# Optimization experiments

Hardware: AMD Instinct MI355X
Metric: run time of the kernel (lower is better)

The kernel has to match this reference:

```python
import jax, jax.numpy as jnp
import numpy as np

D = 1024
H = 16
HD = D // H
EPS = 1e-9


def setup_inputs() -> dict:
    key = jax.random.key(0)
    ks = jax.random.split(key, 16)
    B, Lq, Lk = 8, 512, 1024
    s = 0.02
    return {
        "q": jax.random.normal(ks[0], (B, Lq, D), jnp.float32),
        "q_mask": jnp.ones((B, Lq), jnp.bool_),
        "kv": jax.random.normal(ks[1], (B, Lk, D), jnp.float32),
        "kv_mask": jnp.ones((B, Lk), jnp.bool_),
        # MultiheadAttention packed in-proj + out-proj
        "in_proj_w": jax.random.normal(ks[2], (3 * D, D), jnp.float32) * s,
        "in_proj_b": jnp.zeros((3 * D,), jnp.float32),
        "out_w": jax.random.normal(ks[3], (D, D), jnp.float32) * s,
        "out_b": jnp.zeros((D,), jnp.float32),
        # shared LayerNorm
        "ln_g": jnp.ones((D,), jnp.float32),
        "ln_b": jnp.zeros((D,), jnp.float32),
        # FFN
        "w1": jax.random.normal(ks[4], (4 * D, D), jnp.float32) * s,
        "b1": jnp.zeros((4 * D,), jnp.float32),
        "w2": jax.random.normal(ks[5], (D, 4 * D), jnp.float32) * s,
        "b2": jnp.zeros((D,), jnp.float32),
        # gate MLP
        "gw1": jax.random.normal(ks[6], (D, 2 * D), jnp.float32) * s,
        "gb1": jnp.zeros((D,), jnp.float32),
        "gw2": jax.random.normal(ks[7], (1, D), jnp.float32) * s,
        "gb2": jnp.zeros((1,), jnp.float32),
    }


def _layer_norm(x, g, b, eps=1e-5):
    mu = x.mean(-1, keepdims=True)
    var = ((x - mu) ** 2).mean(-1, keepdims=True)
    return (x - mu) * jax.lax.rsqrt(var + eps) * g + b


def reference(q, q_mask, kv, kv_mask, in_proj_w, in_proj_b, out_w, out_b,
              ln_g, ln_b, w1, b1, w2, b2, gw1, gb1, gw2, gb2):
    B, Lq, _ = q.shape
    Lk = kv.shape[1]
    # packed projections (torch Linear convention: x @ W.T + b)
    qp = (q @ in_proj_w[:D].T + in_proj_b[:D]).reshape(B, Lq, H, HD)
    kp = (kv @ in_proj_w[D:2 * D].T + in_proj_b[D:2 * D]).reshape(B, Lk, H, HD)
    vp = (kv @ in_proj_w[2 * D:].T + in_proj_b[2 * D:]).reshape(B, Lk, H, HD)
    scores = jnp.einsum('bqhd,bkhd->bhqk', qp, kp) / np.sqrt(HD)  # (B,H,Lq,Lk)
    scores = jnp.where(kv_mask[:, None, None, :], scores, -1e30)
    attn = jax.nn.softmax(scores, axis=-1)
    ctx = jnp.einsum('bhqk,bkhd->bqhd', attn, vp).reshape(B, Lq, D)
    attn_out = ctx @ out_w.T + out_b
    # entropy over keys, normalized by log(Lk), averaged over heads
    p = jnp.clip(attn, EPS)
    ent = -(p * jnp.log(p)).sum(-1) / jnp.log(jnp.float32(Lk))  # (B,H,Lq)
    ent = ent.mean(axis=1)[..., None]  # (B,Lq,1)
    conf = jnp.clip(1.0 - ent, 0.0, 1.0)
    # gate MLP on [q, attn_out]
    h = jax.nn.gelu(jnp.concatenate([q, attn_out], -1) @ gw1.T + gb1, approximate=False)
    g = jax.nn.sigmoid(h @ gw2.T + gb2) * conf
    q2 = _layer_norm(q + attn_out * g, ln_g, ln_b)
    ffn = jax.nn.gelu(q2 @ w1.T + b1, approximate=False) @ w2.T + b2
    q2 = _layer_norm(q2 + ffn, ln_g, ln_b)
    return q2, ent
```

## Files before the change

### kernel.cpp

```cpp
#include <hip/hip_runtime.h>
#include <cstdint>
#include <cstddef>

typedef __bf16 bf16;
typedef __bf16 bf16x8 __attribute__((ext_vector_type(8)));
typedef __bf16 bf16x4 __attribute__((ext_vector_type(4)));
typedef float  f32x4  __attribute__((ext_vector_type(4)));

#define GLOAD_LDS16(g, l) __builtin_amdgcn_global_load_lds( \
    (const __attribute__((address_space(1))) unsigned int*)(g), \
    (__attribute__((address_space(3))) unsigned int*)(l), 16, 0, 0)

static constexpr int D_  = 1024;
static constexpr int H_  = 16;
static constexpr int HD_ = 64;
static constexpr int B_  = 8;
static constexpr int LQ_ = 512;
static constexpr int LK_ = 1024;
static constexpr int MQ_ = B_ * LQ_;
static constexpr float LOG2E_ = 1.4426950408889634f;
static constexpr float INV_LN_LK_ = 0.14426950408889634f;
static constexpr float CSHIFT_ = 8.0f;

__device__ __forceinline__ float gelu_f(float v) {
    return 0.5f * v * (1.0f + erff(v * 0.70710678118654752f));
}

__global__ __launch_bounds__(256)
void cast_all_k(const float* __restrict__ ipw, const float* __restrict__ outw,
                const float* __restrict__ w1,  const float* __restrict__ w2,
                const float* __restrict__ gw1, const float* __restrict__ q,
                const float* __restrict__ kv,
                bf16* __restrict__ ipw_b, bf16* __restrict__ outw_b,
                bf16* __restrict__ w1_b,  bf16* __restrict__ w2_b,
                bf16* __restrict__ gw1_b, bf16* __restrict__ x_b,
                bf16* __restrict__ kv_b) {
    const int b = blockIdx.x, t = threadIdx.x;
    const float* src; bf16* dst; long e;
    if (b < 1536)       { src = ipw;  dst = ipw_b;  e = (long)b * 2048; }
    else if (b < 2048)  { src = outw; dst = outw_b; e = (long)(b - 1536) * 2048; }
    else if (b < 4096)  { src = w1;   dst = w1_b;   e = (long)(b - 2048) * 2048; }
    else if (b < 6144)  { src = w2;   dst = w2_b;   e = (long)(b - 4096) * 2048; }
    else if (b < 7168)  { src = gw1;  dst = gw1_b;  e = (long)(b - 6144) * 2048; }
    else if (b < 11264) { src = kv;   dst = kv_b;   e = (long)(b - 7168) * 2048; }
    else {
        long e2 = (long)(b - 11264) * 2048 + t * 8;
        float4 a = *(const float4*)(q + e2);
        float4 c = *(const float4*)(q + e2 + 4);
        bf16x8 o;
        o[0]=(bf16)a.x; o[1]=(bf16)a.y; o[2]=(bf16)a.z; o[3]=(bf16)a.w;
        o[4]=(bf16)c.x; o[5]=(bf16)c.y; o[6]=(bf16)c.z; o[7]=(bf16)c.w;
        long row = e2 >> 10, col = e2 & 1023;
        *(bf16x8*)(x_b + row * 2048 + col) = o;
        return;
    }
    e += t * 8;
    float4 a = *(const float4*)(src + e);
    float4 c = *(const float4*)(src + e + 4);
    bf16x8 o;
    o[0]=(bf16)a.x; o[1]=(bf16)a.y; o[2]=(bf16)a.z; o[3]=(bf16)a.w;
    o[4]=(bf16)c.x; o[5]=(bf16)c.y; o[6]=(bf16)c.z; o[7]=(bf16)c.w;
    *(bf16x8*)(dst + e) = o;
}

template<int ACT, int OUTB, int OUTF>
__device__ __forceinline__
void gemm_body(const bf16* __restrict__ A, int lda,
               const bf16* __restrict__ W, int ldw,
               const float* __restrict__ bias,
               bf16* __restrict__ Cb, int ldcb,
               float* __restrict__ Cf, int ldcf,
               int K) {
    __shared__ __attribute__((aligned(16))) bf16 As[128 * 32];
    __shared__ __attribute__((aligned(16))) bf16 Bs[128 * 32];
    const int gx = gridDim.x;
    const int nwg = gx * gridDim.y;
    const int flat = blockIdx.x + gx * blockIdx.y;
    const int swz = (flat & 7) * (nwg >> 3) + (flat >> 3);
    const int by = swz / gx, bx = swz - by * gx;
    const int t = threadIdx.x;
    const int w = t >> 6, l = t & 63;
    const int l15 = l & 15, lg = l >> 4;
    const int row0 = by * 128, col0 = bx * 128;
    const int wr = (w >> 1) * 64, wc = (w & 1) * 64;

    f32x4 acc[4][4];
#pragma unroll
    for (int m = 0; m < 4; ++m)
#pragma unroll
        for (int n = 0; n < 4; ++n) acc[m][n] = f32x4{0.f, 0.f, 0.f, 0.f};

    const int nk = K >> 5;
    for (int ks = 0; ks < nk; ++ks) {
        __syncthreads();
        const int k0 = ks * 32;
#pragma unroll
        for (int i = 0; i < 2; ++i) {
            int f = i * 256 + t;
            int rr = f >> 2, c8 = (f & 3) * 8;
            GLOAD_LDS16(A + (size_t)(row0 + rr) * lda + k0 + c8,
                        As + (size_t)(i * 256 + w * 64) * 8);
            GLOAD_LDS16(W + (size_t)(col0 + rr) * ldw + k0 + c8,
                        Bs + (size_t)(i * 256 + w * 64) * 8);
        }
        __syncthreads();
        bf16x8 af[4], bfm[4];
#pragma unroll
        for (int m = 0; m < 4; ++m)
            af[m] = *(const bf16x8*)&As[(wr + m * 16 + l15) * 32 + lg * 8];
#pragma unroll
        for (int n = 0; n < 4; ++n)
            bfm[n] = *(const bf16x8*)&Bs[(wc + n * 16 + l15) * 32 + lg * 8];
#pragma unroll
        for (int m = 0; m < 4; ++m)
#pragma unroll
            for (int n = 0; n < 4; ++n)
                acc[m][n] = __builtin_amdgcn_mfma_f32_16x16x32_bf16(af[m], bfm[n], acc[m][n], 0, 0, 0);
    }

#pragma unroll
    for (int n = 0; n < 4; ++n) {
        int gcol = col0 + wc + n * 16 + l15;
        float bv = bias ? bias[gcol] : 0.f;
#pragma unroll
        for (int m = 0; m < 4; ++m) {
            int grow = row0 + wr + m * 16 + lg * 4;
#pragma unroll
            for (int r = 0; r < 4; ++r) {
                float v = acc[m][n][r] + bv;
                if (ACT == 1) v = gelu_f(v);
                if (OUTB) Cb[(size_t)(grow + r) * ldcb + gcol] = (bf16)v;
                if (OUTF) Cf[(size_t)(grow + r) * ldcf + gcol] = v;
            }
        }
    }
}

__device__ __forceinline__
void gemm_splitk_body(const bf16* __restrict__ A, int lda,
                      const bf16* __restrict__ W, int ldw,
                      float* __restrict__ C0, float* __restrict__ C1, int ldcf,
                      int K, int aoff, int woff) {
    __shared__ __attribute__((aligned(16))) bf16 As[128 * 32];
    __shared__ __attribute__((aligned(16))) bf16 Bs[128 * 32];
    const int gx = gridDim.x, gy = gridDim.y;
    const int nwg = gx * gy * gridDim.z;
    const int flat = blockIdx.x + gx * (blockIdx.y + gy * blockIdx.z);
    const int swz = (flat & 7) * (nwg >> 3) + (flat >> 3);
    const int z = swz / (gx * gy);
    const int rem = swz - z * (gx * gy);
    const int by = rem / gx, bx = rem - by * gx;
    A += (size_t)z * aoff;
    W += (size_t)z * woff;
    float* Cf = z ? C1 : C0;

    const int t = threadIdx.x;
    const int w = t >> 6, l = t & 63;
    const int l15 = l & 15, lg = l >> 4;
    const int row0 = by * 128, col0 = bx * 128;
    const int wr = (w >> 1) * 64, wc = (w & 1) * 64;

    f32x4 acc[4][4];
#pragma unroll
    for (int m = 0; m < 4; ++m)
#pragma unroll
        for (int n = 0; n < 4; ++n) acc[m][n] = f32x4{0.f, 0.f, 0.f, 0.f};

    const int nk = K >> 5;
    for (int ks = 0; ks < nk; ++ks) {
        __syncthreads();
        const int k0 = ks * 32;
#pragma unroll
        for (int i = 0; i < 2; ++i) {
            int f = i * 256 + t;
            int rr = f >> 2, c8 = (f & 3) * 8;
            GLOAD_LDS16(A + (size_t)(row0 + rr) * lda + k0 + c8,
                        As + (size_t)(i * 256 + w * 64) * 8);
            GLOAD_LDS16(W + (size_t)(col0 + rr) * ldw + k0 + c8,
                        Bs + (size_t)(i * 256 + w * 64) * 8);
        }
        __syncthreads();
        bf16x8 af[4], bfm[4];
#pragma unroll
        for (int m = 0; m < 4; ++m)
            af[m] = *(const bf16x8*)&As[(wr + m * 16 + l15) * 32 + lg * 8];
#pragma unroll
        for (int n = 0; n < 4; ++n)
            bfm[n] = *(const bf16x8*)&Bs[(wc + n * 16 + l15) * 32 + lg * 8];
#pragma unroll
        for (int m = 0; m < 4; ++m)
#pragma unroll
            for (int n = 0; n < 4; ++n)
                acc[m][n] = __builtin_amdgcn_mfma_f32_16x16x32_bf16(af[m], bfm[n], acc[m][n], 0, 0, 0);
    }

#pragma unroll
    for (int n = 0; n < 4; ++n) {
        int gcol = col0 + wc + n * 16 + l15;
#pragma unroll
        for (int m = 0; m < 4; ++m) {
            int grow = row0 + wr + m * 16 + lg * 4;
#pragma unroll
            for (int r = 0; r < 4; ++r)
                Cf[(size_t)(grow + r) * ldcf + gcol] = acc[m][n][r];
        }
    }
}

__global__ __launch_bounds__(256)
void gemm_qproj_k(const bf16* A, const bf16* W, const float* bias, bf16* Cb) {
    gemm_body<0,1,0>(A, 2048, W, 1024, bias, Cb, 1024, nullptr, 0, 1024);
}
__global__ __launch_bounds__(256)
void gemm_kvproj_k(const bf16* A, const bf16* W, const float* bias, bf16* Cb) {
    gemm_body<0,1,0>(A, 1024, W, 1024, bias, Cb, 2048, nullptr, 0, 1024);
}
__global__ __launch_bounds__(256)
void gemm_outproj_k(const bf16* A, const bf16* W, const float* bias, bf16* Cb) {
    gemm_body<0,1,0>(A, 1024, W, 1024, bias, Cb, 2048, nullptr, 0, 1024);
}
__global__ __launch_bounds__(256)
void gemm_ffn1_k(const bf16* A, const bf16* W, const float* bias, bf16* Cb) {
    gemm_body<1,1,0>(A, 1024, W, 1024, bias, Cb, 4096, nullptr, 0, 1024);
}
__global__ __launch_bounds__(256)
void gemm_gate2_k(const bf16* A, const bf16* W, float* C0, float* C1) {
    gemm_splitk_body(A, 2048, W, 2048, C0, C1, 1024, 1024, 1024, 1024);
}
__global__ __launch_bounds__(256)
void gemm_ffn2_k(const bf16* A, const bf16* W, float* C0, float* C1) {
    gemm_splitk_body(A, 4096, W, 4096, C0, C1, 1024, 2048, 2048, 2048);
}

__device__ __forceinline__ float red16sum(float v) {
    v += __shfl_xor(v, 1, 64);
    v += __shfl_xor(v, 2, 64);
    v += __shfl_xor(v, 4, 64);
    v += __shfl_xor(v, 8, 64);
    return v;
}

__global__ __launch_bounds__(256)
void attn_k(const bf16* __restrict__ Qp, const bf16* __restrict__ KVp,
            bf16* __restrict__ ctx, float* __restrict__ entm) {
    __shared__ __attribute__((aligned(16))) bf16 Ks[64 * 72];
    __shared__ __attribute__((aligned(16))) bf16 Vts[64 * 72];
    __shared__ __attribute__((aligned(16))) bf16 Ps[4][16 * 72];
    const int t = threadIdx.x, w = t >> 6, l = t & 63;
    const int l15 = l & 15, lg = l >> 4;
    const int h = blockIdx.x, b = blockIdx.y, qt = blockIdx.z;
    const int qrow0 = b * LQ_ + qt * 64 + w * 16;

    bf16x8 aq[2];
#pragma unroll
    for (int kk = 0; kk < 2; ++kk)
        aq[kk] = *(const bf16x8*)(Qp + (size_t)(qrow0 + l15) * D_ + h * HD_ + kk * 32 + lg * 8);

    f32x4 o[4];
    float Zp[4], S1p[4];
#pragma unroll
    for (int n = 0; n < 4; ++n) o[n] = f32x4{0.f, 0.f, 0.f, 0.f};
#pragma unroll
    for (int r = 0; r < 4; ++r) { Zp[r] = 0.f; S1p[r] = 0.f; }

    const float K1 = 0.125f * LOG2E_;
    const float K0 = -CSHIFT_ * LOG2E_;

    for (int c = 0; c < LK_ / 64; ++c) {
        __syncthreads();
        const int kbase = b * LK_ + c * 64;
#pragma unroll
        for (int i = 0; i < 2; ++i) {
            int f = i * 256 + t;
            int key = f >> 3, seg = f & 7;
            const bf16* kvrow = KVp + (size_t)(kbase + key) * 2048 + h * HD_ + seg * 8;
            bf16x8 k8 = *(const bf16x8*)kvrow;
            bf16x8 v8 = *(const bf16x8*)(kvrow + 1024);
            *(bf16x8*)&Ks[key * 72 + seg * 8] = k8;
            int vcol = key ^ (seg << 3);
#pragma unroll
            for (int j = 0; j < 8; ++j) Vts[(seg * 8 + j) * 72 + vcol] = v8[j];
        }
        __syncthreads();

        f32x4 s[4];
#pragma unroll
        for (int n = 0; n < 4; ++n) {
            s[n] = f32x4{0.f, 0.f, 0.f, 0.f};
#pragma unroll
            for (int kk = 0; kk < 2; ++kk) {
                bf16x8 bk = *(const bf16x8*)&Ks[(n * 16 + l15) * 72 + kk * 32 + lg * 8];
                s[n] = __builtin_amdgcn_mfma_f32_16x16x32_bf16(aq[kk], bk, s[n], 0, 0, 0);
            }
        }

        float p[4][4];
#pragma unroll
        for (int r = 0; r < 4; ++r) {
#pragma unroll
            for (int n = 0; n < 4; ++n) {
                float sv = s[n][r];
                float pv = exp2f(fmaf(sv, K1, K0));
                p[n][r] = pv;
                Zp[r] += pv;
                S1p[r] = fmaf(pv, sv, S1p[r]);
            }
        }

#pragma unroll
        for (int r = 0; r < 4; ++r)
#pragma unroll
            for (int n = 0; n < 4; ++n)
                Ps[w][(lg * 4 + r) * 72 + ((n ^ lg) << 4) + l15] = (bf16)p[n][r];

        bf16x8 ap[2];
#pragma unroll
        for (int kk = 0; kk < 2; ++kk)
            ap[kk] = *(const bf16x8*)&Ps[w][l15 * 72 + ((kk * 32 + lg * 8) ^ (((l15 >> 2) & 3) << 4))];
#pragma unroll
        for (int n = 0; n < 4; ++n) {
            const int segd = (n * 2 + (l15 >> 3)) & 7;
#pragma unroll
            for (int kk = 0; kk < 2; ++kk) {
                bf16x8 bv = *(const bf16x8*)&Vts[(n * 16 + l15) * 72 + (((kk * 4 + lg) ^ segd) << 3)];
                o[n] = __builtin_amdgcn_mfma_f32_16x16x32_bf16(ap[kk], bv, o[n], 0, 0, 0);
            }
        }
    }

#pragma unroll
    for (int r = 0; r < 4; ++r) {
        float Zr = red16sum(Zp[r]);
        float S1r = red16sum(S1p[r]) * 0.125f;
        float inv = 1.0f / Zr;
        int grow = qrow0 + lg * 4 + r;
#pragma unroll
        for (int n = 0; n < 4; ++n)
            ctx[(size_t)grow * D_ + h * HD_ + n * 16 + l15] = (bf16)(o[n][r] * inv);
        if (l15 == 0) {
            float ent = (CSHIFT_ + logf(Zr) - S1r * inv) * INV_LN_LK_ * (1.0f / 16.0f);
            atomicAdd(&entm[grow], ent);
        }
    }
}

__device__ __forceinline__ float blk_sum(float v, float* sb) {
#pragma unroll
    for (int m = 1; m < 64; m <<= 1) v += __shfl_xor(v, m, 64);
    int w = threadIdx.x >> 6;
    __syncthreads();
    if ((threadIdx.x & 63) == 0) sb[w] = v;
    __syncthreads();
    return sb[0] + sb[1] + sb[2] + sb[3];
}
__device__ __forceinline__ float2 blk_sum2(float2 v, float* sb) {
#pragma unroll
    for (int m = 1; m < 64; m <<= 1) {
        v.x += __shfl_xor(v.x, m, 64);
        v.y += __shfl_xor(v.y, m, 64);
    }
    int w = threadIdx.x >> 6;
    __syncthreads();
    if ((threadIdx.x & 63) == 0) { sb[w * 2] = v.x; sb[w * 2 + 1] = v.y; }
    __syncthreads();
    return make_float2(sb[0] + sb[2] + sb[4] + sb[6], sb[1] + sb[3] + sb[5] + sb[7]);
}

__global__ __launch_bounds__(256)
void gate_ln1_k(const float* __restrict__ qin, const bf16* __restrict__ xb,
                const float* __restrict__ gp0, const float* __restrict__ gp1,
                const float* __restrict__ gb1, const float* __restrict__ gw2,
                const float* __restrict__ gb2, const float* __restrict__ entm,
                const float* __restrict__ lng, const float* __restrict__ lnb,
                float* __restrict__ q2f, bf16* __restrict__ q2b) {
    __shared__ float sb[8];
    const int row = blockIdx.x, t = threadIdx.x, c0 = t * 4;
    float4 p0 = *(const float4*)(gp0 + (size_t)row * D_ + c0);
    float4 p1 = *(const float4*)(gp1 + (size_t)row * D_ + c0);
    float4 hb = *(const float4*)(gb1 + c0);
    float h0 = gelu_f(p0.x + p1.x + hb.x);
    float h1 = gelu_f(p0.y + p1.y + hb.y);
    float h2 = gelu_f(p0.z + p1.z + hb.z);
    float h3 = gelu_f(p0.w + p1.w + hb.w);
    float4 g4 = *(const float4*)(gw2 + c0);
    float dot = h0 * g4.x + h1 * g4.y + h2 * g4.z + h3 * g4.w;
    dot = blk_sum(dot, sb);
    float g = 1.0f / (1.0f + expf(-(dot + gb2[0])));
    float conf = fminf(fmaxf(1.0f - entm[row], 0.0f), 1.0f);
    g *= conf;
    float4 qv = *(const float4*)(qin + (size_t)row * D_ + c0);
    bf16x4 a4 = *(const bf16x4*)(xb + (size_t)row * 2048 + 1024 + c0);
    float y[4] = { qv.x + (float)a4[0] * g, qv.y + (float)a4[1] * g,
                   qv.z + (float)a4[2] * g, qv.w + (float)a4[3] * g };
    float2 ss = blk_sum2(make_float2(y[0] + y[1] + y[2] + y[3],
                                     y[0]*y[0] + y[1]*y[1] + y[2]*y[2] + y[3]*y[3]), sb);
    float mu = ss.x * (1.0f / D_);
    float var = ss.y * (1.0f / D_) - mu * mu;
    float rs = rsqrtf(var + 1e-5f);
    float4 gg = *(const float4*)(lng + c0);
    float4 bb = *(const float4*)(lnb + c0);
    float o0 = (y[0] - mu) * rs * gg.x + bb.x;
    float o1 = (y[1] - mu) * rs * gg.y + bb.y;
    float o2 = (y[2] - mu) * rs * gg.z + bb.z;
    float o3 = (y[3] - mu) * rs * gg.w + bb.w;
    *(float4*)(q2f + (size_t)row * D_ + c0) = make_float4(o0, o1, o2, o3);
    bf16x4 ob; ob[0] = (bf16)o0; ob[1] = (bf16)o1; ob[2] = (bf16)o2; ob[3] = (bf16)o3;
    *(bf16x4*)(q2b + (size_t)row * D_ + c0) = ob;
}

__global__ __launch_bounds__(256)
void ln2_k(const float* __restrict__ q2f, const float* __restrict__ fp0,
           const float* __restrict__ fp1, const float* __restrict__ b2,
           const float* __restrict__ lng, const float* __restrict__ lnb,
           float* __restrict__ outp) {
    __shared__ float sb[8];
    const int row = blockIdx.x, t = threadIdx.x, c0 = t * 4;
    float4 a = *(const float4*)(q2f + (size_t)row * D_ + c0);
    float4 f0 = *(const float4*)(fp0 + (size_t)row * D_ + c0);
    float4 f1 = *(const float4*)(fp1 + (size_t)row * D_ + c0);
    float4 bv = *(const float4*)(b2 + c0);
    float y[4] = { a.x + f0.x + f1.x + bv.x, a.y + f0.y + f1.y + bv.y,
                   a.z + f0.z + f1.z + bv.z, a.w + f0.w + f1.w + bv.w };
    float2 ss = blk_sum2(make_float2(y[0] + y[1] + y[2] + y[3],
                                     y[0]*y[0] + y[1]*y[1] + y[2]*y[2] + y[3]*y[3]), sb);
    float mu = ss.x * (1.0f / D_);
    float var = ss.y * (1.0f / D_) - mu * mu;
    float rs = rsqrtf(var + 1e-5f);
    float4 gg = *(const float4*)(lng + c0);
    float4 bb = *(const float4*)(lnb + c0);
    *(float4*)(outp + (size_t)row * D_ + c0) = make_float4(
        (y[0] - mu) * rs * gg.x + bb.x, (y[1] - mu) * rs * gg.y + bb.y,
        (y[2] - mu) * rs * gg.z + bb.z, (y[3] - mu) * rs * gg.w + bb.w);
}

extern "C" void kernel_launch(void* const* d_in, const int* in_sizes, int n_in,
                              void* d_out, int out_size, void* d_ws, size_t ws_size,
                              hipStream_t stream) {
    (void)in_sizes; (void)n_in; (void)out_size; (void)ws_size;
    const float* q    = (const float*)d_in[0];
    const float* kv   = (const float*)d_in[2];
    const float* ipw  = (const float*)d_in[4];
    const float* ipb  = (const float*)d_in[5];
    const float* outw = (const float*)d_in[6];
    const float* outb = (const float*)d_in[7];
    const float* lng  = (const float*)d_in[8];
    const float* lnb  = (const float*)d_in[9];
    const float* w1   = (const float*)d_in[10];
    const float* b1   = (const float*)d_in[11];
    const float* w2   = (const float*)d_in[12];
    const float* b2   = (const float*)d_in[13];
    const float* gw1  = (const float*)d_in[14];
    const float* gb1  = (const float*)d_in[15];
    const float* gw2  = (const float*)d_in[16];
    const float* gb2  = (const float*)d_in[17];

    char* ws = (char*)d_ws;
    const size_t MB = 1u << 20;
    bf16*  ipw_b  = (bf16*)(ws + 0);
    bf16*  outw_b = (bf16*)(ws + 6 * MB);
    bf16*  w1_b   = (bf16*)(ws + 8 * MB);
    bf16*  w2_b   = (bf16*)(ws + 16 * MB);
    bf16*  gw1_b  = (bf16*)(ws + 24 * MB);
    bf16*  x_b    = (bf16*)(ws + 28 * MB);
    bf16*  kv_b   = (bf16*)(ws + 44 * MB);
    bf16*  Qp     = (bf16*)(ws + 60 * MB);
    bf16*  KVp    = (bf16*)(ws + 68 * MB);
    bf16*  ctx    = (bf16*)(ws + 100 * MB);
    float* gp0    = (float*)(ws + 44 * MB);
    float* gp1    = (float*)(ws + 60 * MB);
    float* q2f    = (float*)(ws + 76 * MB);
    bf16*  q2b    = (bf16*)(ws + 100 * MB);
    bf16*  h1     = (bf16*)(ws + 44 * MB);
    float* fp0    = (float*)(ws + 28 * MB);
    float* fp1    = (float*)(ws + 0);

    float* out  = (float*)d_out;
    float* entm = out + (size_t)MQ_ * D_;

    (void)hipMemsetAsync(entm, 0, (size_t)MQ_ * sizeof(float), stream);

    cast_all_k<<<13312, 256, 0, stream>>>(ipw, outw, w1, w2, gw1, q, kv,
                                          ipw_b, outw_b, w1_b, w2_b, gw1_b, x_b, kv_b);

    gemm_qproj_k<<<dim3(8, 32), 256, 0, stream>>>(x_b, ipw_b, ipb, Qp);
    gemm_kvproj_k<<<dim3(16, 64), 256, 0, stream>>>(kv_b, ipw_b + 1024 * 1024, ipb + 1024, KVp);
    attn_k<<<dim3(H_, B_, LQ_ / 64), 256, 0, stream>>>(Qp, KVp, ctx, entm);
    gemm_outproj_k<<<dim3(8, 32), 256, 0, stream>>>(ctx, outw_b, outb, x_b + 1024);
    gemm_gate2_k<<<dim3(8, 32, 2), 256, 0, stream>>>(x_b, gw1_b, gp0, gp1);
    gate_ln1_k<<<MQ_, 256, 0, stream>>>(q, x_b, gp0, gp1, gb1, gw2, gb2, entm, lng, lnb, q2f, q2b);
    gemm_ffn1_k<<<dim3(32, 32), 256, 0, stream>>>(q2b, w1_b, b1, h1);
    gemm_ffn2_k<<<dim3(8, 32, 2), 256, 0, stream>>>(h1, w2_b, fp0, fp1);
    ln2_k<<<MQ_, 256, 0, stream>>>(q2f, fp0, fp1, b2, lng, lnb, out);
}
```

Baseline: 341.4 us.

## Double-buffer LDS tiles in GEMM bodies to overlap global loads with MFMA

Both the plain and split-K GEMM bodies now use two LDS buffers for A and W tiles. The next K-slice is issued with global_load_lds into the alternate buffer while MFMAs run on the current one, which drops one barrier per iteration. The global pointers are also precomputed outside the loop. This doubles LDS usage per block, which may reduce occupancy, and correctness depends on the single remaining barrier ordering both the reads and the async writes.

```diff
diff --git a/kernel.cpp b/kernel.cpp
--- a/kernel.cpp
+++ b/kernel.cpp
@@ -71,8 +71,8 @@
                bf16* __restrict__ Cb, int ldcb,
                float* __restrict__ Cf, int ldcf,
                int K) {
-    __shared__ __attribute__((aligned(16))) bf16 As[128 * 32];
-    __shared__ __attribute__((aligned(16))) bf16 Bs[128 * 32];
+    __shared__ __attribute__((aligned(16))) bf16 As[2][128 * 32];
+    __shared__ __attribute__((aligned(16))) bf16 Bs[2][128 * 32];
     const int gx = gridDim.x;
     const int nwg = gx * gridDim.y;
     const int flat = blockIdx.x + gx * blockIdx.y;
@@ -84,6 +84,13 @@
     const int row0 = by * 128, col0 = bx * 128;
     const int wr = (w >> 1) * 64, wc = (w & 1) * 64;
 
+    const int f1 = 256 + t;
+    const bf16* gA0 = A + (size_t)(row0 + (t >> 2)) * lda + (t & 3) * 8;
+    const bf16* gW0 = W + (size_t)(col0 + (t >> 2)) * ldw + (t & 3) * 8;
+    const bf16* gA1 = A + (size_t)(row0 + (f1 >> 2)) * lda + (f1 & 3) * 8;
+    const bf16* gW1 = W + (size_t)(col0 + (f1 >> 2)) * ldw + (f1 & 3) * 8;
+    const int doff = w * 512;
+
     f32x4 acc[4][4];
 #pragma unroll
     for (int m = 0; m < 4; ++m)
@@ -91,31 +98,39 @@
         for (int n = 0; n < 4; ++n) acc[m][n] = f32x4{0.f, 0.f, 0.f, 0.f};
 
     const int nk = K >> 5;
+    GLOAD_LDS16(gA0, (bf16*)As[0] + doff);
+    GLOAD_LDS16(gW0, (bf16*)Bs[0] + doff);
+    GLOAD_LDS16(gA1, (bf16*)As[0] + doff + 2048);
+    GLOAD_LDS16(gW1, (bf16*)Bs[0] + doff + 2048);
+    __syncthreads();
+
+    int cur = 0;
     for (int ks = 0; ks < nk; ++ks) {
-        __syncthreads();
-        const int k0 = ks * 32;
-#pragma unroll
-        for (int i = 0; i < 2; ++i) {
-            int f = i * 256 + t;
-            int rr = f >> 2, c8 = (f & 3) * 8;
-            GLOAD_LDS16(A + (size_t)(row0 + rr) * lda + k0 + c8,
-                        As + (size_t)(i * 256 + w * 64) * 8);
-            GLOAD_LDS16(W + (size_t)(col0 + rr) * ldw + k0 + c8,
-                        Bs + (size_t)(i * 256 + w * 64) * 8);
-        }
-        __syncthreads();
+        const bf16* Ac = As[cur];
+        const bf16* Bc = Bs[cur];
         bf16x8 af[4], bfm[4];
 #pragma unroll
         for (int m = 0; m < 4; ++m)
-            af[m] = *(const bf16x8*)&As[(wr + m * 16 + l15) * 32 + lg * 8];
+            af[m] = *(const bf16x8*)&Ac[(wr + m * 16 + l15) * 32 + lg * 8];
 #pragma unroll
         for (int n = 0; n < 4; ++n)
-            bfm[n] = *(const bf16x8*)&Bs[(wc + n * 16 + l15) * 32 + lg * 8];
+            bfm[n] = *(const bf16x8*)&Bc[(wc + n * 16 + l15) * 32 + lg * 8];
+        if (ks + 1 < nk) {
+            const int k0 = (ks + 1) * 32;
+            bf16* dA = (bf16*)As[cur ^ 1] + doff;
+            bf16* dB = (bf16*)Bs[cur ^ 1] + doff;
+            GLOAD_LDS16(gA0 + k0, dA);
+            GLOAD_LDS16(gW0 + k0, dB);
+            GLOAD_LDS16(gA1 + k0, dA + 2048);
+            GLOAD_LDS16(gW1 + k0, dB + 2048);
+        }
 #pragma unroll
         for (int m = 0; m < 4; ++m)
 #pragma unroll
             for (int n = 0; n < 4; ++n)
                 acc[m][n] = __builtin_amdgcn_mfma_f32_16x16x32_bf16(af[m], bfm[n], acc[m][n], 0, 0, 0);
+        __syncthreads();
+        cur ^= 1;
     }
 
 #pragma unroll
@@ -141,8 +156,8 @@
                       const bf16* __restrict__ W, int ldw,
                       float* __restrict__ C0, float* __restrict__ C1, int ldcf,
                       int K, int aoff, int woff) {
-    __shared__ __attribute__((aligned(16))) bf16 As[128 * 32];
-    __shared__ __attribute__((aligned(16))) bf16 Bs[128 * 32];
+    __shared__ __attribute__((aligned(16))) bf16 As[2][128 * 32];
+    __shared__ __attribute__((aligned(16))) bf16 Bs[2][128 * 32];
     const int gx = gridDim.x, gy = gridDim.y;
     const int nwg = gx * gy * gridDim.z;
     const int flat = blockIdx.x + gx * (blockIdx.y + gy * blockIdx.z);
@@ -160,6 +175,13 @@
     const int row0 = by * 128, col0 = bx * 128;
     const int wr = (w >> 1) * 64, wc = (w & 1) * 64;
 
+    const int f1 = 256 + t;
+    const bf16* gA0 = A + (size_t)(row0 + (t >> 2)) * lda + (t & 3) * 8;
+    const bf16* gW0 = W + (size_t)(col0 + (t >> 2)) * ldw + (t & 3) * 8;
+    const bf16* gA1 = A + (size_t)(row0 + (f1 >> 2)) * lda + (f1 & 3) * 8;
+    const bf16* gW1 = W + (size_t)(col0 + (f1 >> 2)) * ldw + (f1 & 3) * 8;
+    const int doff = w * 512;
+
     f32x4 acc[4][4];
 #pragma unroll
     for (int m = 0; m < 4; ++m)
@@ -167,31 +189,39 @@
         for (int n = 0; n < 4; ++n) acc[m][n] = f32x4{0.f, 0.f, 0.f, 0.f};
 
     const int nk = K >> 5;
+    GLOAD_LDS16(gA0, (bf16*)As[0] + doff);
+    GLOAD_LDS16(gW0, (bf16*)Bs[0] + doff);
+    GLOAD_LDS16(gA1, (bf16*)As[0] + doff + 2048);
+    GLOAD_LDS16(gW1, (bf16*)Bs[0] + doff + 2048);
+    __syncthreads();
+
+    int cur = 0;
     for (int ks = 0; ks < nk; ++ks) {
-        __syncthreads();
-        const int k0 = ks * 32;
-#pragma unroll
-        for (int i = 0; i < 2; ++i) {
-            int f = i * 256 + t;
-            int rr = f >> 2, c8 = (f & 3) * 8;
-            GLOAD_LDS16(A + (size_t)(row0 + rr) * lda + k0 + c8,
-                        As + (size_t)(i * 256 + w * 64) * 8);
-            GLOAD_LDS16(W + (size_t)(col0 + rr) * ldw + k0 + c8,
-                        Bs + (size_t)(i * 256 + w * 64) * 8);
-        }
-        __syncthreads();
+        const bf16* Ac = As[cur];
+        const bf16* Bc = Bs[cur];
         bf16x8 af[4], bfm[4];
 #pragma unroll
         for (int m = 0; m < 4; ++m)
-            af[m] = *(const bf16x8*)&As[(wr + m * 16 + l15) * 32 + lg * 8];
+            af[m] = *(const bf16x8*)&Ac[(wr + m * 16 + l15) * 32 + lg * 8];
 #pragma unroll
         for (int n = 0; n < 4; ++n)
-            bfm[n] = *(const bf16x8*)&Bs[(wc + n * 16 + l15) * 32 + lg * 8];
+            bfm[n] = *(const bf16x8*)&Bc[(wc + n * 16 + l15) * 32 + lg * 8];
+        if (ks + 1 < nk) {
+            const int k0 = (ks + 1) * 32;
+            bf16* dA = (bf16*)As[cur ^ 1] + doff;
+            bf16* dB = (bf16*)Bs[cur ^ 1] + doff;
+            GLOAD_LDS16(gA0 + k0, dA);
+            GLOAD_LDS16(gW0 + k0, dB);
+            GLOAD_LDS16(gA1 + k0, dA + 2048);
+            GLOAD_LDS16(gW1 + k0, dB + 2048);
+        }
 #pragma unroll
         for (int m = 0; m < 4; ++m)
 #pragma unroll
             for (int n = 0; n < 4; ++n)
                 acc[m][n] = __builtin_amdgcn_mfma_f32_16x16x32_bf16(af[m], bfm[n], acc[m][n], 0, 0, 0);
+        __syncthreads();
+        cur ^= 1;
     }
 
 #pragma unroll
```

Result: slower. 352.5 us (+3.2%).

## Add 256x256-tile double-buffered GEMM for KV projection and FFN1

Applied to the files above, without the earlier changes.

Adds a new GEMM kernel with 256x256 output tiles, K-step 64, 512 threads and double-buffered LDS filled by direct global-to-LDS loads with an XOR swizzle. It replaces the 128x128 GEMM for the KV projection and the first FFN layer. The bigger tiles raise arithmetic intensity and cut global traffic per FLOP. The cost is 128KB of LDS and a large accumulator footprint, which limits occupancy, and a smaller grid (256 workgroups) that may fill the CUs unevenly.

```diff
diff --git a/kernel.cpp b/kernel.cpp
--- a/kernel.cpp
+++ b/kernel.cpp
@@ -63,6 +63,112 @@
     *(bf16x8*)(dst + e) = o;
 }
 
+template<int ACT>
+__device__ __forceinline__
+void gemm256_body(const bf16* __restrict__ A, int lda,
+                  const bf16* __restrict__ W, int ldw,
+                  const float* __restrict__ bias,
+                  bf16* __restrict__ Cb, int ldcb, int K) {
+    __shared__ __attribute__((aligned(16))) bf16 As[2][256 * 64];
+    __shared__ __attribute__((aligned(16))) bf16 Bs[2][256 * 64];
+    const int gx = gridDim.x;
+    const int nwg = gx * gridDim.y;
+    const int flat = blockIdx.x + gx * blockIdx.y;
+    const int swzb = (flat & 7) * (nwg >> 3) + (flat >> 3);
+    const int by = swzb / gx, bx = swzb - by * gx;
+    const int t = threadIdx.x;
+    const int w = t >> 6, l = t & 63, l15 = l & 15, lg = l >> 4;
+    const int wr = w >> 2, wc = w & 3;
+    const int row0 = by * 256, col0 = bx * 256;
+    const int sw = l15 & 7;
+
+    size_t aoff[4], woff[4];
+    int ldsoff[4];
+#pragma unroll
+    for (int j = 0; j < 4; ++j) {
+        int id = j * 512 + t;
+        int r = id >> 3, c = id & 7;
+        aoff[j] = (size_t)(row0 + r) * lda + ((c ^ (r & 7)) << 3);
+        woff[j] = (size_t)(col0 + r) * ldw + ((c ^ (r & 7)) << 3);
+        ldsoff[j] = (j * 512 + w * 64) * 8;
+    }
+
+    f32x4 acc[8][4];
+#pragma unroll
+    for (int m = 0; m < 8; ++m)
+#pragma unroll
+        for (int n = 0; n < 4; ++n) acc[m][n] = f32x4{0.f, 0.f, 0.f, 0.f};
+
+    const int nt = K >> 6;
+#pragma unroll
+    for (int j = 0; j < 4; ++j) {
+        GLOAD_LDS16(A + aoff[j], (bf16*)As[0] + ldsoff[j]);
+        GLOAD_LDS16(W + woff[j], (bf16*)Bs[0] + ldsoff[j]);
+    }
+    __syncthreads();
+
+    for (int kt = 0; kt < nt; ++kt) {
+        const int cur = kt & 1;
+        if (kt + 1 < nt) {
+            const size_t k0 = (size_t)(kt + 1) * 64;
+            bf16* dA = (bf16*)As[cur ^ 1];
+            bf16* dB = (bf16*)Bs[cur ^ 1];
+#pragma unroll
+            for (int j = 0; j < 4; ++j) {
+                GLOAD_LDS16(A + aoff[j] + k0, dA + ldsoff[j]);
+                GLOAD_LDS16(W + woff[j] + k0, dB + ldsoff[j]);
+            }
+        }
+        const bf16* Ac = As[cur];
+        const bf16* Bc = Bs[cur];
+#pragma unroll
+        for (int ks2 = 0; ks2 < 2; ++ks2) {
+            bf16x8 af[8], bfr[4];
+#pragma unroll
+            for (int m = 0; m < 8; ++m) {
+                int ra = wr * 128 + m * 16 + l15;
+                af[m] = *(const bf16x8*)&Ac[ra * 64 + (((ks2 * 4 + lg) ^ sw) << 3)];
+            }
+#pragma unroll
+            for (int n = 0; n < 4; ++n) {
+                int rb = wc * 64 + n * 16 + l15;
+                bfr[n] = *(const bf16x8*)&Bc[rb * 64 + (((ks2 * 4 + lg) ^ sw) << 3)];
+            }
+#pragma unroll
+            for (int m = 0; m < 8; ++m)
+#pragma unroll
+                for (int n = 0; n < 4; ++n)
+                    acc[m][n] = __builtin_amdgcn_mfma_f32_16x16x32_bf16(af[m], bfr[n], acc[m][n], 0, 0, 0);
+        }
+        __syncthreads();
+    }
+
+#pragma unroll
+    for (int n = 0; n < 4; ++n) {
+        int gcol = col0 + wc * 64 + n * 16 + l15;
+        float bv = bias[gcol];
+#pragma unroll
+        for (int m = 0; m < 8; ++m) {
+            int grow = row0 + wr * 128 + m * 16 + lg * 4;
+#pragma unroll
+            for (int r = 0; r < 4; ++r) {
+                float v = acc[m][n][r] + bv;
+                if (ACT) v = gelu_f(v);
+                Cb[(size_t)(grow + r) * ldcb + gcol] = (bf16)v;
+            }
+        }
+    }
+}
+
+__global__ __launch_bounds__(512, 2)
+void gemm256_kvproj_k(const bf16* A, const bf16* W, const float* bias, bf16* Cb) {
+    gemm256_body<0>(A, 1024, W, 1024, bias, Cb, 2048, 1024);
+}
+__global__ __launch_bounds__(512, 2)
+void gemm256_ffn1_k(const bf16* A, const bf16* W, const float* bias, bf16* Cb) {
+    gemm256_body<1>(A, 1024, W, 1024, bias, Cb, 4096, 1024);
+}
+
 template<int ACT, int OUTB, int OUTF>
 __device__ __forceinline__
 void gemm_body(const bf16* __restrict__ A, int lda,
@@ -212,16 +318,8 @@
     gemm_body<0,1,0>(A, 2048, W, 1024, bias, Cb, 1024, nullptr, 0, 1024);
 }
 __global__ __launch_bounds__(256)
-void gemm_kvproj_k(const bf16* A, const bf16* W, const float* bias, bf16* Cb) {
-    gemm_body<0,1,0>(A, 1024, W, 1024, bias, Cb, 2048, nullptr, 0, 1024);
-}
-__global__ __launch_bounds__(256)
 void gemm_outproj_k(const bf16* A, const bf16* W, const float* bias, bf16* Cb) {
     gemm_body<0,1,0>(A, 1024, W, 1024, bias, Cb, 2048, nullptr, 0, 1024);
-}
-__global__ __launch_bounds__(256)
-void gemm_ffn1_k(const bf16* A, const bf16* W, const float* bias, bf16* Cb) {
-    gemm_body<1,1,0>(A, 1024, W, 1024, bias, Cb, 4096, nullptr, 0, 1024);
 }
 __global__ __launch_bounds__(256)
 void gemm_gate2_k(const bf16* A, const bf16* W, float* C0, float* C1) {
@@ -483,12 +581,12 @@
                                           ipw_b, outw_b, w1_b, w2_b, gw1_b, x_b, kv_b);
 
     gemm_qproj_k<<<dim3(8, 32), 256, 0, stream>>>(x_b, ipw_b, ipb, Qp);
-    gemm_kvproj_k<<<dim3(16, 64), 256, 0, stream>>>(kv_b, ipw_b + 1024 * 1024, ipb + 1024, KVp);
+    gemm256_kvproj_k<<<dim3(8, 32), 512, 0, stream>>>(kv_b, ipw_b + 1024 * 1024, ipb + 1024, KVp);
     attn_k<<<dim3(H_, B_, LQ_ / 64), 256, 0, stream>>>(Qp, KVp, ctx, entm);
     gemm_outproj_k<<<dim3(8, 32), 256, 0, stream>>>(ctx, outw_b, outb, x_b + 1024);
     gemm_gate2_k<<<dim3(8, 32, 2), 256, 0, stream>>>(x_b, gw1_b, gp0, gp1);
     gate_ln1_k<<<MQ_, 256, 0, stream>>>(q, x_b, gp0, gp1, gb1, gw2, gb2, entm, lng, lnb, q2f, q2b);
-    gemm_ffn1_k<<<dim3(32, 32), 256, 0, stream>>>(q2b, w1_b, b1, h1);
+    gemm256_ffn1_k<<<dim3(16, 16), 512, 0, stream>>>(q2b, w1_b, b1, h1);
     gemm_ffn2_k<<<dim3(8, 32, 2), 256, 0, stream>>>(h1, w2_b, fp0, fp1);
     ln2_k<<<MQ_, 256, 0, stream>>>(q2f, fp0, fp1, b2, lng, lnb, out);
 }
```

Measured after the change: 314.9 us. 7.8% less time.

## Use 128x256 tile GEMM with 512 threads for KV-proj and FFN1

Applied to the files above, without the earlier changes.

Adds a new GEMM kernel with 128x256 output tiles, 8 waves, double-buffered direct-to-LDS loads and an LDS-staged, vectorized bf16 epilogue. The KV projection and FFN1 GEMMs switch to it, halving the grid and raising reuse of the A tile across more columns. This trades per-block register and LDS footprint and fewer blocks for higher arithmetic intensity and coalesced stores.

```diff
diff --git a/kernel.cpp b/kernel.cpp
--- a/kernel.cpp
+++ b/kernel.cpp
@@ -63,6 +63,109 @@
     *(bf16x8*)(dst + e) = o;
 }
 
+template<int ACT>
+__device__ __forceinline__
+void gemm128x256_body(const bf16* __restrict__ A, int lda,
+                      const bf16* __restrict__ W, int ldw,
+                      const float* __restrict__ bias,
+                      bf16* __restrict__ Cb, int ldcb, int K) {
+    __shared__ __attribute__((aligned(16))) bf16 LDSb[2][12288];
+    const int gx = gridDim.x;
+    const int nwg = gx * gridDim.y;
+    const int flat = blockIdx.x + gx * blockIdx.y;
+    const int swz = (flat & 7) * (nwg >> 3) + (flat >> 3);
+    const int by = swz / gx, bx = swz - by * gx;
+    const int t = threadIdx.x;
+    const int w = t >> 6, l = t & 63, l15 = l & 15, lg = l >> 4;
+    const int wrr = w >> 2, wc = w & 3;
+    const int row0 = by * 128, col0 = bx * 256;
+    const int sw = l15 & 3;
+
+    const int trow = t >> 2;
+    const int scol = ((t & 3) ^ (trow & 3)) << 3;
+    const bf16* pA  = A + (size_t)(row0 + trow) * lda + scol;
+    const bf16* pB0 = W + (size_t)(col0 + trow) * ldw + scol;
+    const bf16* pB1 = W + (size_t)(col0 + 128 + trow) * ldw + scol;
+    const int ldsoA  = w * 512;
+    const int ldsoB0 = 4096 + w * 512;
+    const int ldsoB1 = 8192 + w * 512;
+
+    f32x4 acc[4][4];
+#pragma unroll
+    for (int m = 0; m < 4; ++m)
+#pragma unroll
+        for (int n = 0; n < 4; ++n) acc[m][n] = f32x4{0.f, 0.f, 0.f, 0.f};
+
+    const int nk = K >> 5;
+    GLOAD_LDS16(pA,  (bf16*)LDSb[0] + ldsoA);
+    GLOAD_LDS16(pB0, (bf16*)LDSb[0] + ldsoB0);
+    GLOAD_LDS16(pB1, (bf16*)LDSb[0] + ldsoB1);
+
+    for (int kt = 0; kt < nk; ++kt) {
+        const int cur = kt & 1;
+        if (kt + 1 < nk) {
+            const int kc = (kt + 1) * 32;
+            bf16* d = (bf16*)LDSb[cur ^ 1];
+            GLOAD_LDS16(pA + kc,  d + ldsoA);
+            GLOAD_LDS16(pB0 + kc, d + ldsoB0);
+            GLOAD_LDS16(pB1 + kc, d + ldsoB1);
+            asm volatile("s_waitcnt vmcnt(3)" ::: "memory");
+        } else {
+            asm volatile("s_waitcnt vmcnt(0)" ::: "memory");
+        }
+        __builtin_amdgcn_s_barrier();
+        const bf16* bufA = (const bf16*)LDSb[cur];
+        const bf16* bufB = bufA + 4096;
+        const int kcol = (lg ^ sw) << 3;
+        bf16x8 bf4[4];
+#pragma unroll
+        for (int n = 0; n < 4; ++n)
+            bf4[n] = *(const bf16x8*)&bufB[(wc * 64 + n * 16 + l15) * 32 + kcol];
+#pragma unroll
+        for (int m = 0; m < 4; ++m) {
+            bf16x8 afm = *(const bf16x8*)&bufA[(wrr * 64 + m * 16 + l15) * 32 + kcol];
+#pragma unroll
+            for (int n = 0; n < 4; ++n)
+                acc[m][n] = __builtin_amdgcn_mfma_f32_16x16x32_bf16(afm, bf4[n], acc[m][n], 0, 0, 0);
+        }
+        __builtin_amdgcn_s_barrier();
+    }
+
+    float bvn[4];
+#pragma unroll
+    for (int n = 0; n < 4; ++n) bvn[n] = bias[col0 + wc * 64 + n * 16 + l15];
+    const int erow = l >> 2, ec = (l & 3) * 16;
+#pragma unroll
+    for (int m = 0; m < 4; ++m) {
+        bf16* ep = (bf16*)LDSb + ((m & 1) * 8 + w) * 1152;
+#pragma unroll
+        for (int n = 0; n < 4; ++n)
+#pragma unroll
+            for (int r = 0; r < 4; ++r) {
+                float v = acc[m][n][r] + bvn[n];
+                if (ACT) v = gelu_f(v);
+                ep[(lg * 4 + r) * 72 + n * 16 + l15] = (bf16)v;
+            }
+        asm volatile("s_waitcnt lgkmcnt(0)" ::: "memory");
+        __builtin_amdgcn_sched_barrier(0);
+        bf16x8 v8a = *(const bf16x8*)&ep[erow * 72 + ec];
+        bf16x8 v8b = *(const bf16x8*)&ep[erow * 72 + ec + 8];
+        const int grow = row0 + wrr * 64 + m * 16 + erow;
+        bf16* dst = Cb + (size_t)grow * ldcb + col0 + wc * 64 + ec;
+        *(bf16x8*)dst = v8a;
+        *(bf16x8*)(dst + 8) = v8b;
+    }
+}
+
+__global__ __launch_bounds__(512, 4)
+void gemmA_kvproj_k(const bf16* A, const bf16* W, const float* bias, bf16* Cb) {
+    gemm128x256_body<0>(A, 1024, W, 1024, bias, Cb, 2048, 1024);
+}
+__global__ __launch_bounds__(512, 4)
+void gemmA_ffn1_k(const bf16* A, const bf16* W, const float* bias, bf16* Cb) {
+    gemm128x256_body<1>(A, 1024, W, 1024, bias, Cb, 4096, 1024);
+}
+
 template<int ACT, int OUTB, int OUTF>
 __device__ __forceinline__
 void gemm_body(const bf16* __restrict__ A, int lda,
@@ -212,16 +315,8 @@
     gemm_body<0,1,0>(A, 2048, W, 1024, bias, Cb, 1024, nullptr, 0, 1024);
 }
 __global__ __launch_bounds__(256)
-void gemm_kvproj_k(const bf16* A, const bf16* W, const float* bias, bf16* Cb) {
-    gemm_body<0,1,0>(A, 1024, W, 1024, bias, Cb, 2048, nullptr, 0, 1024);
-}
-__global__ __launch_bounds__(256)
 void gemm_outproj_k(const bf16* A, const bf16* W, const float* bias, bf16* Cb) {
     gemm_body<0,1,0>(A, 1024, W, 1024, bias, Cb, 2048, nullptr, 0, 1024);
-}
-__global__ __launch_bounds__(256)
-void gemm_ffn1_k(const bf16* A, const bf16* W, const float* bias, bf16* Cb) {
-    gemm_body<1,1,0>(A, 1024, W, 1024, bias, Cb, 4096, nullptr, 0, 1024);
 }
 __global__ __launch_bounds__(256)
 void gemm_gate2_k(const bf16* A, const bf16* W, float* C0, float* C1) {
@@ -483,12 +578,12 @@
                                           ipw_b, outw_b, w1_b, w2_b, gw1_b, x_b, kv_b);
 
     gemm_qproj_k<<<dim3(8, 32), 256, 0, stream>>>(x_b, ipw_b, ipb, Qp);
-    gemm_kvproj_k<<<dim3(16, 64), 256, 0, stream>>>(kv_b, ipw_b + 1024 * 1024, ipb + 1024, KVp);
+    gemmA_kvproj_k<<<dim3(8, 64), 512, 0, stream>>>(kv_b, ipw_b + 1024 * 1024, ipb + 1024, KVp);
     attn_k<<<dim3(H_, B_, LQ_ / 64), 256, 0, stream>>>(Qp, KVp, ctx, entm);
     gemm_outproj_k<<<dim3(8, 32), 256, 0, stream>>>(ctx, outw_b, outb, x_b + 1024);
     gemm_gate2_k<<<dim3(8, 32, 2), 256, 0, stream>>>(x_b, gw1_b, gp0, gp1);
     gate_ln1_k<<<MQ_, 256, 0, stream>>>(q, x_b, gp0, gp1, gb1, gw2, gb2, entm, lng, lnb, q2f, q2b);
-    gemm_ffn1_k<<<dim3(32, 32), 256, 0, stream>>>(q2b, w1_b, b1, h1);
+    gemmA_ffn1_k<<<dim3(16, 32), 512, 0, stream>>>(q2b, w1_b, b1, h1);
     gemm_ffn2_k<<<dim3(8, 32, 2), 256, 0, stream>>>(h1, w2_b, fp0, fp1);
     ln2_k<<<MQ_, 256, 0, stream>>>(q2f, fp0, fp1, b2, lng, lnb, out);
 }
```

Measured after the change: 322.5 us. 1.06x faster.
